# Optimization experiments

Measured on AMD Instinct MI355X. Metric: run time of the kernel, lower is better.

The kernel has to match this reference:

```python
import jax, jax.numpy as jnp
import numpy as np

B, CIN, IMG = 8, 512, 112
P = IMG // 14          # patch_size = 8
NP = 14 * 14           # n_patch = 196
DEC, SKIP, EMB = 512, 512, 768
BN_EPS = 1e-3          # keras BatchNormalization default
IN_EPS = 1e-3          # tfa InstanceNormalization default


def conv2d(x, w, b, stride=1):
    # x: NCHW, w: OIHW
    y = jax.lax.conv_general_dilated(x, w, (stride, stride), 'VALID',
                                     dimension_numbers=('NCHW', 'OIHW', 'NCHW'))
    return y + b[None, :, None, None]


def bn_inf(x, g, b, m, v):
    scale = g / jnp.sqrt(v + BN_EPS)
    return (x - m[None, :, None, None]) * scale[None, :, None, None] + b[None, :, None, None]


def setup_inputs() -> dict:
    key = jax.random.key(0)
    ks = jax.random.split(key, 20)
    s = 0.05
    return {
        'decoder': jax.random.normal(ks[0], (B, CIN, IMG, IMG), jnp.float32),
        'trans': jax.random.normal(ks[1], (B, NP, EMB), jnp.float32),
        'pe_w': jax.random.normal(ks[2], (DEC, CIN, P, P), jnp.float32) * s,
        'pe_b': jax.random.normal(ks[3], (DEC,), jnp.float32) * s,
        'mc_w': jax.random.normal(ks[4], (SKIP, CIN, 1, 1), jnp.float32) * s,
        'mc_b': jax.random.normal(ks[5], (SKIP,), jnp.float32) * s,
        'bn1_g': jax.random.uniform(ks[6], (SKIP,), jnp.float32, 0.5, 1.5),
        'bn1_b': jax.random.normal(ks[7], (SKIP,), jnp.float32) * s,
        'bn1_m': jax.random.normal(ks[8], (SKIP,), jnp.float32) * s,
        'bn1_v': jax.random.uniform(ks[9], (SKIP,), jnp.float32, 0.5, 1.5),
        'wq': jax.random.normal(ks[10], (DEC, SKIP), jnp.float32) * s,
        'wk': jax.random.normal(ks[11], (EMB, SKIP), jnp.float32) * s,
        'wv': jax.random.normal(ks[12], (EMB, SKIP), jnp.float32) * s,
        'wo': jax.random.normal(ks[13], (SKIP, SKIP), jnp.float32) * s,
        'psi_g': jnp.ones((1,), jnp.float32),
        'psi_b': jnp.zeros((1,), jnp.float32),
        'rc_w': jax.random.normal(ks[14], (SKIP, SKIP, 1, 1), jnp.float32) * s,
        'rc_b': jax.random.normal(ks[15], (SKIP,), jnp.float32) * s,
        'bn2_g': jax.random.uniform(ks[16], (SKIP,), jnp.float32, 0.5, 1.5),
        'bn2_b': jax.random.normal(ks[17], (SKIP,), jnp.float32) * s,
        'bn2_m': jax.random.normal(ks[18], (SKIP,), jnp.float32) * s,
        'bn2_v': jax.random.uniform(ks[19], (SKIP,), jnp.float32, 0.5, 1.5),
    }


def reference(decoder, trans, pe_w, pe_b, mc_w, mc_b, bn1_g, bn1_b, bn1_m, bn1_v,
              wq, wk, wv, wo, psi_g, psi_b, rc_w, rc_b, bn2_g, bn2_b, bn2_m, bn2_v):
    # mask branch: 1x1 conv + BN + ReLU  -> [B, SKIP, IMG, IMG]
    mask = jax.nn.relu(bn_inf(conv2d(decoder, mc_w, mc_b), bn1_g, bn1_b, bn1_m, bn1_v))

    # patch embedding: strided conv -> [B, DEC, 14, 14] -> tokens [B, NP, DEC]
    dl = conv2d(decoder, pe_w, pe_b, stride=P)
    dl = dl.reshape(dl.shape[0], dl.shape[1], -1).transpose(0, 2, 1)

    q = jnp.einsum('bnd,ds->bsn', dl, wq)       # [B, SKIP, NP]
    k = jnp.einsum('bne,es->bns', trans, wk)    # [B, NP, SKIP]
    v = jnp.einsum('bne,es->bsn', trans, wv)    # [B, SKIP, NP]

    sim = jnp.einsum('bsn,bnt->bst', q, k)      # [B, SKIP, SKIP]
    # InstanceNorm over the (SKIP, SKIP) map per sample (single channel)
    mu = sim.mean(axis=(1, 2), keepdims=True)
    var = sim.var(axis=(1, 2), keepdims=True)
    sim = (sim - mu) / jnp.sqrt(var + IN_EPS) * psi_g[0] + psi_b[0]
    sim = jax.nn.softmax(sim, axis=-1)

    out = jnp.einsum('bst,btn->bns', sim, v)    # [B, NP, SKIP]
    out = jnp.einsum('bns,so->bno', out, wo)    # [B, NP, SKIP]

    # reconstruct: tokens -> [B, SKIP, 14, 14] -> nearest upsample x P -> 1x1 conv + BN + ReLU
    x = out.transpose(0, 2, 1).reshape(out.shape[0], SKIP, 14, 14)
    x = jnp.repeat(jnp.repeat(x, P, axis=2), P, axis=3)
    x = jax.nn.relu(bn_inf(conv2d(x, rc_w, rc_b), bn2_g, bn2_b, bn2_m, bn2_v))

    return x * mask
```

## Files before the change

### kernel.cpp

```cpp
#include <hip/hip_runtime.h>
#include <stdint.h>

typedef __attribute__((ext_vector_type(8))) short v8s;
typedef __attribute__((ext_vector_type(4))) float v4f;

__device__ __forceinline__ uint16_t f2bf(float x){
  uint32_t u = __float_as_uint(x);
  return (uint16_t)((u + 0x7FFFu + ((u >> 16) & 1u)) >> 16);
}
__device__ __forceinline__ uint32_t pk2(float a, float b){
  return (uint32_t)f2bf(a) | ((uint32_t)f2bf(b) << 16);
}
__device__ __forceinline__ int swz(int e){ return e ^ (((e >> 7) & 3) << 3); }

__device__ __forceinline__ void gl16(const uint16_t* g, uint16_t* l){
  __builtin_amdgcn_global_load_lds((const __attribute__((address_space(1))) void*)g,
                                   (__attribute__((address_space(3))) void*)l, 16, 0, 0);
}

__global__ void __launch_bounds__(256) dra_cvt(const float* __restrict__ s,
                                               uint16_t* __restrict__ d, int n8){
  int i = blockIdx.x * 256 + threadIdx.x;
  if (i >= n8) return;
  const float4* sp = (const float4*)(s + (size_t)i * 8);
  float4 f0 = sp[0], f1 = sp[1];
  uint4 u; u.x = pk2(f0.x, f0.y); u.y = pk2(f0.z, f0.w);
  u.z = pk2(f1.x, f1.y); u.w = pk2(f1.z, f1.w);
  *(uint4*)(d + (size_t)i * 8) = u;
}

__global__ void __launch_bounds__(256) dra_tcvt(const float* __restrict__ s,
                                                uint16_t* __restrict__ d, int R, int C){
  int r8 = R >> 3;
  int id = blockIdx.x * 256 + threadIdx.x;
  if (id >= C * r8) return;
  int c = id / r8, r0 = (id - c * r8) * 8;
  float v[8];
  #pragma unroll
  for (int e = 0; e < 8; e++) v[e] = s[(size_t)(r0 + e) * C + c];
  uint4 u; u.x = pk2(v[0], v[1]); u.y = pk2(v[2], v[3]);
  u.z = pk2(v[4], v[5]); u.w = pk2(v[6], v[7]);
  *(uint4*)(d + (size_t)c * R + r0) = u;
}

__global__ void __launch_bounds__(256) dra_tdec(const float* __restrict__ dec,
                                                uint16_t* __restrict__ decT){
  __shared__ uint16_t lt[64 * 80];
  int t = threadIdx.x;
  int pos0 = blockIdx.x * 64;
  int ci0  = blockIdx.y * 64;
  int b    = blockIdx.z;
  #pragma unroll
  for (int i = 0; i < 4; i++){
    int idx = t + i * 256;
    int ci_l = idx >> 4, p4 = (idx & 15) * 4;
    const float4 f = *(const float4*)(dec + ((size_t)(b * 512 + ci0 + ci_l)) * 12544 + pos0 + p4);
    lt[(p4 + 0) * 80 + ci_l] = f2bf(f.x);
    lt[(p4 + 1) * 80 + ci_l] = f2bf(f.y);
    lt[(p4 + 2) * 80 + ci_l] = f2bf(f.z);
    lt[(p4 + 3) * 80 + ci_l] = f2bf(f.w);
  }
  __syncthreads();
  #pragma unroll
  for (int i = 0; i < 2; i++){
    int idx = t + i * 256;
    int p_l = idx >> 3, u = idx & 7;
    uint4 v = *(const uint4*)&lt[p_l * 80 + u * 8];
    *(uint4*)(decT + ((size_t)b * 12544 + pos0 + p_l) * 512 + ci0 + u * 8) = v;
  }
}

__global__ void __launch_bounds__(256) dra_wpe2(const float* __restrict__ pw,
                                                uint16_t* __restrict__ w2){
  int id = blockIdx.x * 256 + threadIdx.x;
  if (id >= 2097152) return;
  int co = id >> 12, rem = id & 4095;
  int ci8 = rem >> 6, pix = rem & 63;
  const float* s = pw + (size_t)co * 32768 + ci8 * 512 + pix;
  float v[8];
  #pragma unroll
  for (int j = 0; j < 8; j++) v[j] = s[j * 64];
  uint4 u; u.x = pk2(v[0], v[1]); u.y = pk2(v[2], v[3]);
  u.z = pk2(v[4], v[5]); u.w = pk2(v[6], v[7]);
  *(uint4*)(w2 + (size_t)co * 32768 + pix * 512 + ci8 * 8) = u;
}

__global__ void __launch_bounds__(256) dra_transb(const float* __restrict__ tr,
                                                  uint16_t* __restrict__ d){
  int id = blockIdx.x * 256 + threadIdx.x;
  if (id >= 1792 * 96) return;
  int n = id / 96, e0 = (id - n * 96) * 8;
  int b = n / 224, nl = n - b * 224;
  uint4 u = {0u,0u,0u,0u};
  if (nl < 196){
    const float* sp = tr + ((size_t)(b * 196 + nl)) * 768 + e0;
    u.x = pk2(sp[0], sp[1]); u.y = pk2(sp[2], sp[3]);
    u.z = pk2(sp[4], sp[5]); u.w = pk2(sp[6], sp[7]);
  }
  *(uint4*)(d + (size_t)n * 768 + e0) = u;
}

__global__ void dra_scales(const float* mcb, const float* g1, const float* b1,
                           const float* m1, const float* v1,
                           const float* rcb, const float* g2, const float* b2,
                           const float* m2, const float* v2,
                           float* s1, float* o1, float* s2, float* o2){
  int i = blockIdx.x * 256 + threadIdx.x;
  if (i >= 512) return;
  float sc1 = g1[i] / sqrtf(v1[i] + 1e-3f);
  s1[i] = sc1; o1[i] = (mcb[i] - m1[i]) * sc1 + b1[i];
  float sc2 = g2[i] / sqrtf(v2[i] + 1e-3f);
  s2[i] = sc2; o2[i] = (rcb[i] - m2[i]) * sc2 + b2[i];
}

__global__ void __launch_bounds__(256, 4) dra_k1(const uint16_t* __restrict__ decT,
    const uint16_t* __restrict__ wpe2, float* __restrict__ part)
{
  __shared__ uint16_t lA[128 * 32];
  __shared__ uint16_t lB[128 * 32];
  int t = threadIdx.x;
  int L = blockIdx.x;
  int x = L & 7, n = L >> 3;
  int shi = n / 56, rem = n - shi * 56;
  int tok_t = rem >> 2, co_t = rem & 3;
  int s    = shi * 8 + x;
  int bco  = co_t * 128;
  int tok0 = tok_t * 128;
  int lane = t & 63, w = t >> 6;
  int wm = w >> 1, wn = w & 1;
  int lr = lane & 15, lg = lane >> 4;

  const uint16_t* aB[2]; const uint16_t* bB[2]; int uu[2];
  #pragma unroll
  for (int i = 0; i < 2; i++){
    int u = t + i * 256; uu[i] = u;
    int row = u >> 2, h = u & 3;
    int token = tok0 + row;
    int b = token / 224, tl = token - b * 224;
    if (tl > 195) tl = 195;
    int py = tl / 14, px = tl - py * 14;
    aB[i] = decT + ((size_t)b * 12544 + py * 896 + px * 8) * 512 + h * 8;
    bB[i] = wpe2 + (size_t)(bco + row) * 32768 + h * 8;
  }

  const v4f vzero = {0.f,0.f,0.f,0.f};
  v4f acc[4][4];
  #pragma unroll
  for (int i = 0; i < 4; i++)
    #pragma unroll
    for (int j = 0; j < 4; j++) acc[i][j] = vzero;

  for (int pix = s * 4; pix < s * 4 + 4; ++pix){
    int ky = pix >> 3, kx = pix & 7;
    int poff = (ky * 112 + kx) * 512;
    int k0p  = pix * 512;
    for (int ci0 = 0; ci0 < 512; ci0 += 32){
      gl16(aB[0] + poff + ci0, &lA[uu[0] * 8]);
      gl16(aB[1] + poff + ci0, &lA[uu[1] * 8]);
      gl16(bB[0] + k0p + ci0,  &lB[uu[0] * 8]);
      gl16(bB[1] + k0p + ci0,  &lB[uu[1] * 8]);
      __syncthreads();
      v8s av[4], bv[4];
      #pragma unroll
      for (int mf = 0; mf < 4; mf++) av[mf] = *(const v8s*)&lA[(wm*64 + mf*16 + lr) * 32 + lg * 8];
      #pragma unroll
      for (int nf = 0; nf < 4; nf++) bv[nf] = *(const v8s*)&lB[(wn*64 + nf*16 + lr) * 32 + lg * 8];
      #pragma unroll
      for (int mf = 0; mf < 4; mf++)
        #pragma unroll
        for (int nf = 0; nf < 4; nf++)
          acc[mf][nf] = __builtin_amdgcn_mfma_f32_16x16x32_bf16(av[mf], bv[nf], acc[mf][nf], 0, 0, 0);
      __syncthreads();
    }
  }

  float* pd = part + (size_t)s * 917504;
  #pragma unroll
  for (int mf = 0; mf < 4; mf++){
    #pragma unroll
    for (int nf = 0; nf < 4; nf++){
      int tokg = tok0 + wm*64 + mf*16 + lg*4;
      int cog  = bco  + wn*64 + nf*16 + lr;
      #pragma unroll
      for (int r = 0; r < 4; r++)
        pd[(size_t)(tokg + r) * 512 + cog] = acc[mf][nf][r];
    }
  }
}

__global__ void __launch_bounds__(256) dra_red(const float* __restrict__ part,
    const float* __restrict__ peb, uint16_t* __restrict__ dlb){
  int id = blockIdx.x * 256 + threadIdx.x;
  if (id >= 114688) return;
  int tok = id >> 6, c8 = (id & 63) * 8;
  float a0=0,a1=0,a2=0,a3=0,a4=0,a5=0,a6=0,a7=0;
  #pragma unroll
  for (int s = 0; s < 16; s++){
    const float* p = part + (size_t)s * 917504 + (size_t)tok * 512 + c8;
    float4 x = *(const float4*)p, y = *(const float4*)(p + 4);
    a0 += x.x; a1 += x.y; a2 += x.z; a3 += x.w;
    a4 += y.x; a5 += y.y; a6 += y.z; a7 += y.w;
  }
  const float4 b0 = *(const float4*)(peb + c8), b1 = *(const float4*)(peb + c8 + 4);
  uint4 o; o.x = pk2(a0 + b0.x, a1 + b0.y); o.y = pk2(a2 + b0.z, a3 + b0.w);
  o.z = pk2(a4 + b1.x, a5 + b1.y); o.w = pk2(a6 + b1.z, a7 + b1.w);
  *(uint4*)(dlb + (size_t)tok * 512 + c8) = o;
}

template<int MREP>
__global__ void __launch_bounds__(256, 2) dra_gemm(
    const uint16_t* __restrict__ A, const uint16_t* __restrict__ Bn, void* __restrict__ Dv,
    int M, int N, int K, int lda, int ldb, int ldd,
    long long sAz, long long sBz, long long sDz,
    int epi, const float* __restrict__ svec, const float* __restrict__ ovec)
{
  constexpr int BM = MREP * 32;
  __shared__ uint16_t lA[BM * 32];
  __shared__ uint16_t lB[64 * 32];
  int t = threadIdx.x, z = blockIdx.z;
  int bm = blockIdx.x * BM, bn = blockIdx.y * 64;
  const uint16_t* Az = A + (size_t)z * sAz;
  const uint16_t* Bz = Bn + (size_t)z * sBz;
  int lane = t & 63, w = t >> 6;
  int wm = w >> 1, wn = w & 1;
  int lr = lane & 15, lg = lane >> 4;
  const v4f vzero = {0.f, 0.f, 0.f, 0.f};
  v4f acc[MREP][2];
  #pragma unroll
  for (int i = 0; i < MREP; i++){ acc[i][0] = vzero; acc[i][1] = vzero; }

  for (int k0 = 0; k0 < K; k0 += 32){
    #pragma unroll
    for (int i = 0; i < MREP/2; i++){
      int idx = t + i * 256;
      int r = idx >> 2, ko = (idx & 3) << 3;
      int rg = bm + r; if (rg >= M) rg = M - 1;
      *(uint4*)&lA[swz(r * 32 + ko)] = *(const uint4*)(Az + (size_t)rg * lda + k0 + ko);
    }
    {
      int r = t >> 2, ko = (t & 3) << 3;
      *(uint4*)&lB[swz(r * 32 + ko)] = *(const uint4*)(Bz + (size_t)(bn + r) * ldb + k0 + ko);
    }
    __syncthreads();
    v8s av[MREP], bv[2];
    #pragma unroll
    for (int mf = 0; mf < MREP; mf++)
      av[mf] = *(const v8s*)&lA[swz((wm*(MREP*16) + mf*16 + lr) * 32 + lg * 8)];
    #pragma unroll
    for (int nf = 0; nf < 2; nf++)
      bv[nf] = *(const v8s*)&lB[swz((wn*32 + nf*16 + lr) * 32 + lg * 8)];
    #pragma unroll
    for (int mf = 0; mf < MREP; mf++)
      #pragma unroll
      for (int nf = 0; nf < 2; nf++)
        acc[mf][nf] = __builtin_amdgcn_mfma_f32_16x16x32_bf16(av[mf], bv[nf], acc[mf][nf], 0, 0, 0);
    __syncthreads();
  }

  #pragma unroll
  for (int mf = 0; mf < MREP; mf++){
    #pragma unroll
    for (int nf = 0; nf < 2; nf++){
      int mg0 = bm + wm*(MREP*16) + mf*16 + lg*4;
      int ng  = bn + wn*32 + nf*16 + lr;
      #pragma unroll
      for (int r = 0; r < 4; r++){
        int mg = mg0 + r;
        if (mg < M){
          float val = acc[mf][nf][r];
          size_t di = (size_t)z * sDz + (size_t)mg * ldd + ng;
          if (epi == 0)      ((float*)Dv)[di] = val;
          else if (epi == 1) ((uint16_t*)Dv)[di] = f2bf(val);
          else ((float*)Dv)[di] = fmaxf(val * svec[mg] + ovec[mg], 0.f);
        }
      }
    }
  }
}

__global__ void __launch_bounds__(256) dra_stats1(const float* __restrict__ sim,
                                                  double* __restrict__ ps){
  __shared__ double d1[256], d2[256];
  int b = blockIdx.y, blk = blockIdx.x, t = threadIdx.x;
  const float* s = sim + (size_t)b * 262144 + (size_t)blk * 2048 + t * 8;
  float4 x = *(const float4*)s, y = *(const float4*)(s + 4);
  double p1 = (double)x.x + x.y + x.z + x.w + y.x + y.y + y.z + y.w;
  double p2 = (double)x.x*x.x + (double)x.y*x.y + (double)x.z*x.z + (double)x.w*x.w
            + (double)y.x*y.x + (double)y.y*y.y + (double)y.z*y.z + (double)y.w*y.w;
  d1[t] = p1; d2[t] = p2;
  __syncthreads();
  for (int o = 128; o > 0; o >>= 1){
    if (t < o){ d1[t] += d1[t + o]; d2[t] += d2[t + o]; }
    __syncthreads();
  }
  if (t == 0){
    ps[(b * 128 + blk) * 2 + 0] = d1[0];
    ps[(b * 128 + blk) * 2 + 1] = d2[0];
  }
}

__global__ void __launch_bounds__(128) dra_stats2(const double* __restrict__ ps,
    const float* __restrict__ psig, const float* __restrict__ psib, float* __restrict__ ac){
  __shared__ double d1[128], d2[128];
  int b = blockIdx.x, t = threadIdx.x;
  d1[t] = ps[(b * 128 + t) * 2 + 0];
  d2[t] = ps[(b * 128 + t) * 2 + 1];
  __syncthreads();
  for (int o = 64; o > 0; o >>= 1){
    if (t < o){ d1[t] += d1[t + o]; d2[t] += d2[t + o]; }
    __syncthreads();
  }
  if (t == 0){
    double mean = d1[0] * (1.0 / 262144.0);
    double var  = d2[0] * (1.0 / 262144.0) - mean * mean;
    float a = psig[0] / (float)sqrt(var + 1e-3);
    ac[b * 2 + 0] = a;
    ac[b * 2 + 1] = psib[0] - (float)mean * a;
  }
}

__global__ void __launch_bounds__(256) dra_soft(const float* __restrict__ sim,
    const float* __restrict__ ac, uint16_t* __restrict__ P){
  int srow = blockIdx.x, b = blockIdx.y, t = threadIdx.x;
  const float* row = sim + (size_t)b * 262144 + (size_t)srow * 512;
  float a = ac[b * 2], c = ac[b * 2 + 1];
  float v0 = row[t] * a + c, v1 = row[t + 256] * a + c;
  __shared__ float red[256];
  red[t] = fmaxf(v0, v1);
  __syncthreads();
  for (int o = 128; o > 0; o >>= 1){
    if (t < o) red[t] = fmaxf(red[t], red[t + o]);
    __syncthreads();
  }
  float m = red[0];
  __syncthreads();
  float e0 = __expf(v0 - m), e1 = __expf(v1 - m);
  red[t] = e0 + e1;
  __syncthreads();
  for (int o = 128; o > 0; o >>= 1){
    if (t < o) red[t] += red[t + o];
    __syncthreads();
  }
  float inv = 1.f / red[0];
  uint16_t* pr = P + (size_t)b * 262144 + (size_t)srow * 512;
  pr[t] = f2bf(e0 * inv); pr[t + 256] = f2bf(e1 * inv);
}

__global__ void __launch_bounds__(256, 4) dra_k3(const uint16_t* __restrict__ decT,
    const uint16_t* __restrict__ mcw, const float* __restrict__ s1,
    const float* __restrict__ o1, const float* __restrict__ recon,
    float* __restrict__ outp)
{
  __shared__ uint16_t lA[128 * 32];
  __shared__ uint16_t lB[128 * 32];
  int t = threadIdx.x;
  int L = blockIdx.x;
  int x = L & 7, n = L >> 3;
  int co_t = n & 3, pg = n >> 2;
  int p = pg * 8 + x;
  int bz = p / 98, pt = p - bz * 98;
  int bco  = co_t * 128;
  int pos0 = pt * 128;
  int lane = t & 63, w = t >> 6;
  int wm = w >> 1, wn = w & 1;
  int lr = lane & 15, lg = lane >> 4;

  const uint16_t* aB[2]; const uint16_t* bB[2]; int uu[2];
  #pragma unroll
  for (int i = 0; i < 2; i++){
    int u = t + i * 256; uu[i] = u;
    int row = u >> 2, h = u & 3;
    aB[i] = mcw  + (size_t)(bco + row) * 512 + h * 8;
    bB[i] = decT + ((size_t)bz * 12544 + pos0 + row) * 512 + h * 8;
  }

  const v4f vzero = {0.f,0.f,0.f,0.f};
  v4f acc[4][4];
  #pragma unroll
  for (int i = 0; i < 4; i++)
    #pragma unroll
    for (int j = 0; j < 4; j++) acc[i][j] = vzero;

  for (int k0 = 0; k0 < 512; k0 += 32){
    gl16(aB[0] + k0, &lA[uu[0] * 8]);
    gl16(aB[1] + k0, &lA[uu[1] * 8]);
    gl16(bB[0] + k0, &lB[uu[0] * 8]);
    gl16(bB[1] + k0, &lB[uu[1] * 8]);
    __syncthreads();
    v8s av[4], bv[4];
    #pragma unroll
    for (int mf = 0; mf < 4; mf++) av[mf] = *(const v8s*)&lA[(wm*64 + mf*16 + lr) * 32 + lg * 8];
    #pragma unroll
    for (int nf = 0; nf < 4; nf++) bv[nf] = *(const v8s*)&lB[(wn*64 + nf*16 + lr) * 32 + lg * 8];
    #pragma unroll
    for (int mf = 0; mf < 4; mf++)
      #pragma unroll
      for (int nf = 0; nf < 4; nf++)
        acc[mf][nf] = __builtin_amdgcn_mfma_f32_16x16x32_bf16(av[mf], bv[nf], acc[mf][nf], 0, 0, 0);
    __syncthreads();
  }

  #pragma unroll
  for (int mf = 0; mf < 4; mf++){
    #pragma unroll
    for (int r = 0; r < 4; r++){
      int co = bco + wm*64 + mf*16 + lg*4 + r;
      float sc = s1[co], of = o1[co];
      const float* rrow = recon + (size_t)co * 1792 + bz * 224;
      #pragma unroll
      for (int nf = 0; nf < 4; nf++){
        int pos = pos0 + wn*64 + nf*16 + lr;
        int h = pos / 112, wd = pos - h * 112;
        int pcol = (h >> 3) * 14 + (wd >> 3);
        float mask = fmaxf(acc[mf][nf][r] * sc + of, 0.f);
        outp[((size_t)(bz * 512 + co)) * 12544 + pos] = mask * rrow[pcol];
      }
    }
  }
}

extern "C" void kernel_launch(void* const* d_in, const int* in_sizes, int n_in,
                              void* d_out, int out_size, void* d_ws, size_t ws_size,
                              hipStream_t stream) {
  (void)in_sizes; (void)n_in; (void)out_size; (void)ws_size;
  const float* dec   = (const float*)d_in[0];
  const float* trans = (const float*)d_in[1];
  const float* pe_w  = (const float*)d_in[2];
  const float* pe_b  = (const float*)d_in[3];
  const float* mc_w  = (const float*)d_in[4];
  const float* mc_b  = (const float*)d_in[5];
  const float* bn1g  = (const float*)d_in[6];
  const float* bn1b  = (const float*)d_in[7];
  const float* bn1m  = (const float*)d_in[8];
  const float* bn1v  = (const float*)d_in[9];
  const float* wq    = (const float*)d_in[10];
  const float* wk    = (const float*)d_in[11];
  const float* wv    = (const float*)d_in[12];
  const float* wo    = (const float*)d_in[13];
  const float* psig  = (const float*)d_in[14];
  const float* psib  = (const float*)d_in[15];
  const float* rc_w  = (const float*)d_in[16];
  const float* rc_b  = (const float*)d_in[17];
  const float* bn2g  = (const float*)d_in[18];
  const float* bn2b  = (const float*)d_in[19];
  const float* bn2m  = (const float*)d_in[20];
  const float* bn2v  = (const float*)d_in[21];

  char* p = (char*)d_ws;
  auto take = [&](size_t bytes) -> void* {
    void* r = (void*)p; p += (bytes + 255) & ~(size_t)255; return r;
  };
  uint16_t* decT   = (uint16_t*)take((size_t)8 * 12544 * 512 * 2);
  uint16_t* wpe2   = (uint16_t*)take((size_t)512 * 32768 * 2);
  uint16_t* mcw    = (uint16_t*)take((size_t)512 * 512 * 2);
  uint16_t* rcw    = (uint16_t*)take((size_t)512 * 512 * 2);
  uint16_t* wqT    = (uint16_t*)take((size_t)512 * 512 * 2);
  uint16_t* woT    = (uint16_t*)take((size_t)512 * 512 * 2);
  uint16_t* wkT    = (uint16_t*)take((size_t)512 * 768 * 2);
  uint16_t* wvT    = (uint16_t*)take((size_t)512 * 768 * 2);
  uint16_t* transb = (uint16_t*)take((size_t)1792 * 768 * 2);
  float*    s1v    = (float*)take(512 * 4);
  float*    o1v    = (float*)take(512 * 4);
  float*    s2v    = (float*)take(512 * 4);
  float*    o2v    = (float*)take(512 * 4);
  uint16_t* dlb    = (uint16_t*)take((size_t)1792 * 512 * 2);
  uint16_t* Qt     = (uint16_t*)take((size_t)512 * 1792 * 2);
  uint16_t* Kt     = (uint16_t*)take((size_t)512 * 1792 * 2);
  uint16_t* Vb     = (uint16_t*)take((size_t)1792 * 512 * 2);
  float*    ac     = (float*)take(256);
  double*   ps     = (double*)take((size_t)8 * 128 * 2 * 8);
  float*    part   = (float*)take((size_t)16 * 1792 * 512 * 4);
  float*    simb   = part;
  uint16_t* P      = (uint16_t*)(part + 2097152);
  uint16_t* outb   = P + 2097152;
  uint16_t* out2   = outb + 917504;
  float*    recon  = (float*)(out2 + 917504);

  dra_tdec<<<dim3(196, 8, 8), 256, 0, stream>>>(dec, decT);
  dra_wpe2<<<8192, 256, 0, stream>>>(pe_w, wpe2);
  dra_cvt<<<128, 256, 0, stream>>>(mc_w, mcw, 32768);
  dra_cvt<<<128, 256, 0, stream>>>(rc_w, rcw, 32768);
  dra_tcvt<<<128, 256, 0, stream>>>(wq, wqT, 512, 512);
  dra_tcvt<<<192, 256, 0, stream>>>(wk, wkT, 768, 512);
  dra_tcvt<<<192, 256, 0, stream>>>(wv, wvT, 768, 512);
  dra_tcvt<<<128, 256, 0, stream>>>(wo, woT, 512, 512);
  dra_transb<<<672, 256, 0, stream>>>(trans, transb);
  dra_scales<<<2, 256, 0, stream>>>(mc_b, bn1g, bn1b, bn1m, bn1v,
                                    rc_b, bn2g, bn2b, bn2m, bn2v, s1v, o1v, s2v, o2v);

  dra_k1<<<896, 256, 0, stream>>>(decT, wpe2, part);
  dra_red<<<448, 256, 0, stream>>>(part, pe_b, dlb);

  dra_gemm<2><<<dim3(8, 28, 1), 256, 0, stream>>>(wqT, dlb, Qt, 512, 1792, 512,
      512, 512, 1792, 0, 0, 0, 1, nullptr, nullptr);
  dra_gemm<2><<<dim3(8, 28, 1), 256, 0, stream>>>(wkT, transb, Kt, 512, 1792, 768,
      768, 768, 1792, 0, 0, 0, 1, nullptr, nullptr);
  dra_gemm<2><<<dim3(28, 8, 1), 256, 0, stream>>>(transb, wvT, Vb, 1792, 512, 768,
      768, 768, 512, 0, 0, 0, 1, nullptr, nullptr);

  dra_gemm<2><<<dim3(8, 8, 8), 256, 0, stream>>>(Qt, Kt, simb, 512, 512, 224,
      1792, 1792, 512, 224, 224, 262144, 0, nullptr, nullptr);
  dra_stats1<<<dim3(128, 8), 256, 0, stream>>>(simb, ps);
  dra_stats2<<<8, 128, 0, stream>>>(ps, psig, psib, ac);
  dra_soft<<<dim3(512, 8), 256, 0, stream>>>(simb, ac, P);

  dra_gemm<2><<<dim3(4, 8, 8), 256, 0, stream>>>(Vb, P, outb, 224, 512, 512,
      512, 512, 512, 114688, 262144, 114688, 1, nullptr, nullptr);
  dra_gemm<2><<<dim3(28, 8, 1), 256, 0, stream>>>(outb, woT, out2, 1792, 512, 512,
      512, 512, 512, 0, 0, 0, 1, nullptr, nullptr);
  dra_gemm<2><<<dim3(8, 28, 1), 256, 0, stream>>>(rcw, out2, recon, 512, 1792, 512,
      512, 512, 1792, 0, 0, 0, 2, s2v, o2v);

  dra_k3<<<3136, 256, 0, stream>>>(decT, mcw, s1v, o1v, recon, (float*)d_out);
}
```

Measured before the change: 432.7 us.

## Enlarge dra_k3 tile to 256x256 with double-buffered LDS and swizzle

The final mask GEMM plus epilogue kernel now uses 512-thread blocks computing 256x256 output tiles instead of 128x128, which halves redundant global reads of A and B per output. LDS is double-buffered so the next K-slice loads while MFMAs run on the current one, removing one barrier per iteration. An XOR swizzle on the 16-byte chunks reduces LDS bank conflicts. In exchange, each wave holds 32 accumulators, which raises register pressure and lowers occupancy, and the grid shrinks to 784 blocks.

Result: slower. 465.3 us (+7.5%).

```diff
diff --git a/kernel.cpp b/kernel.cpp
--- a/kernel.cpp
+++ b/kernel.cpp
@@ -173,7 +173,6 @@
       __syncthreads();
     }
   }
-
   float* pd = part + (size_t)s * 917504;
   #pragma unroll
   for (int mf = 0; mf < 4; mf++){
@@ -346,65 +345,86 @@
   pr[t] = f2bf(e0 * inv); pr[t + 256] = f2bf(e1 * inv);
 }
 
-__global__ void __launch_bounds__(256, 4) dra_k3(const uint16_t* __restrict__ decT,
+__global__ void __launch_bounds__(512, 2) dra_k3(const uint16_t* __restrict__ decT,
     const uint16_t* __restrict__ mcw, const float* __restrict__ s1,
     const float* __restrict__ o1, const float* __restrict__ recon,
     float* __restrict__ outp)
 {
-  __shared__ uint16_t lA[128 * 32];
-  __shared__ uint16_t lB[128 * 32];
+  __shared__ uint16_t lA[2][256 * 32];
+  __shared__ uint16_t lB[2][256 * 32];
   int t = threadIdx.x;
   int L = blockIdx.x;
   int x = L & 7, n = L >> 3;
-  int co_t = n & 3, pg = n >> 2;
-  int p = pg * 8 + x;
-  int bz = p / 98, pt = p - bz * 98;
-  int bco  = co_t * 128;
-  int pos0 = pt * 128;
+  int co_t = n & 1, q = n >> 1;
+  int g = q * 8 + x;
+  int bz = g / 49, pt = g - bz * 49;
+  int bco  = co_t * 256;
+  int pos0 = pt * 256;
   int lane = t & 63, w = t >> 6;
-  int wm = w >> 1, wn = w & 1;
+  int wm = w >> 2, wn = w & 3;
   int lr = lane & 15, lg = lane >> 4;
 
   const uint16_t* aB[2]; const uint16_t* bB[2]; int uu[2];
   #pragma unroll
   for (int i = 0; i < 2; i++){
-    int u = t + i * 256; uu[i] = u;
-    int row = u >> 2, h = u & 3;
-    aB[i] = mcw  + (size_t)(bco + row) * 512 + h * 8;
-    bB[i] = decT + ((size_t)bz * 12544 + pos0 + row) * 512 + h * 8;
+    int u = t + i * 512; uu[i] = u;
+    int row = u >> 2, c = u & 3;
+    int cs = c ^ ((row >> 1) & 3);
+    aB[i] = mcw  + (size_t)(bco + row) * 512 + cs * 8;
+    bB[i] = decT + ((size_t)bz * 12544 + pos0 + row) * 512 + cs * 8;
   }
 
   const v4f vzero = {0.f,0.f,0.f,0.f};
-  v4f acc[4][4];
-  #pragma unroll
-  for (int i = 0; i < 4; i++)
+  v4f acc[8][4];
+  #pragma unroll
+  for (int i = 0; i < 8; i++)
     #pragma unroll
     for (int j = 0; j < 4; j++) acc[i][j] = vzero;
 
-  for (int k0 = 0; k0 < 512; k0 += 32){
-    gl16(aB[0] + k0, &lA[uu[0] * 8]);
-    gl16(aB[1] + k0, &lA[uu[1] * 8]);
-    gl16(bB[0] + k0, &lB[uu[0] * 8]);
-    gl16(bB[1] + k0, &lB[uu[1] * 8]);
-    __syncthreads();
-    v8s av[4], bv[4];
-    #pragma unroll
-    for (int mf = 0; mf < 4; mf++) av[mf] = *(const v8s*)&lA[(wm*64 + mf*16 + lr) * 32 + lg * 8];
-    #pragma unroll
-    for (int nf = 0; nf < 4; nf++) bv[nf] = *(const v8s*)&lB[(wn*64 + nf*16 + lr) * 32 + lg * 8];
-    #pragma unroll
-    for (int mf = 0; mf < 4; mf++)
+  auto stage = [&](int kk, int db){
+    int ko = kk << 5;
+    gl16(aB[0] + ko, &lA[db][uu[0] * 8]);
+    gl16(aB[1] + ko, &lA[db][uu[1] * 8]);
+    gl16(bB[0] + ko, &lB[db][uu[0] * 8]);
+    gl16(bB[1] + ko, &lB[db][uu[1] * 8]);
+  };
+
+  int aoff[8], boff[4];
+  #pragma unroll
+  for (int mf = 0; mf < 8; mf++){
+    int R = wm*128 + mf*16 + lr;
+    aoff[mf] = R * 32 + (lg ^ ((R >> 1) & 3)) * 8;
+  }
+  #pragma unroll
+  for (int nf = 0; nf < 4; nf++){
+    int R = wn*64 + nf*16 + lr;
+    boff[nf] = R * 32 + (lg ^ ((R >> 1) & 3)) * 8;
+  }
+
+  stage(0, 0);
+  __syncthreads();
+  int cur = 0;
+  for (int kk = 0; kk < 16; ++kk){
+    if (kk + 1 < 16) stage(kk + 1, cur ^ 1);
+    v8s av[8], bv[4];
+    #pragma unroll
+    for (int mf = 0; mf < 8; mf++) av[mf] = *(const v8s*)&lA[cur][aoff[mf]];
+    #pragma unroll
+    for (int nf = 0; nf < 4; nf++) bv[nf] = *(const v8s*)&lB[cur][boff[nf]];
+    #pragma unroll
+    for (int mf = 0; mf < 8; mf++)
       #pragma unroll
       for (int nf = 0; nf < 4; nf++)
         acc[mf][nf] = __builtin_amdgcn_mfma_f32_16x16x32_bf16(av[mf], bv[nf], acc[mf][nf], 0, 0, 0);
     __syncthreads();
-  }
-
-  #pragma unroll
-  for (int mf = 0; mf < 4; mf++){
+    cur ^= 1;
+  }
+
+  #pragma unroll
+  for (int mf = 0; mf < 8; mf++){
     #pragma unroll
     for (int r = 0; r < 4; r++){
-      int co = bco + wm*64 + mf*16 + lg*4 + r;
+      int co = bco + wm*128 + mf*16 + lg*4 + r;
       float sc = s1[co], of = o1[co];
       const float* rrow = recon + (size_t)co * 1792 + bz * 224;
       #pragma unroll
@@ -511,5 +531,5 @@
   dra_gemm<2><<<dim3(8, 28, 1), 256, 0, stream>>>(rcw, out2, recon, 512, 1792, 512,
       512, 512, 1792, 0, 0, 0, 2, s2v, o2v);
 
-  dra_k3<<<3136, 256, 0, stream>>>(decT, mcw, s1v, o1v, recon, (float*)d_out);
-}
+  dra_k3<<<784, 512, 0, stream>>>(decT, mcw, s1v, o1v, recon, (float*)d_out);
+}
```
